# Optimization experiments

Measured on AMD Instinct MI355X. Metric: run time of the kernel, lower is better.

The kernel has to match this reference:

```python
import jax, jax.numpy as jnp
import numpy as np

N = 50000
D = 64
K_POS = 32
K_NEG = 64


def setup_inputs() -> dict:
    key = jax.random.key(0)
    ks = jax.random.split(key, 7)
    return {
        "P": jax.random.normal(ks[0], (N, D), dtype=jnp.float32),
        "W_d": jax.random.normal(ks[1], (D,), dtype=jnp.float32),
        "deg_vec": jax.random.uniform(ks[2], (N,), dtype=jnp.float32),
        "pos_idx": jax.random.randint(ks[3], (N, K_POS), 0, N, dtype=jnp.int32),
        "neg_idx": jax.random.randint(ks[4], (N, K_NEG), 0, N, dtype=jnp.int32),
        "deg_pos_idx": jax.random.randint(ks[5], (N, K_POS), 0, N, dtype=jnp.int32),
        "deg_neg_idx": jax.random.randint(ks[6], (N, K_NEG), 0, N, dtype=jnp.int32),
    }


def _contrast(Z, pos, neg):
    # hamming_dist(zi, zp) = sum_d |zi - zp|  (per node i over its index list)
    Hp = jnp.abs(Z[:, None, :] - Z[pos]).sum(-1)  # [N, K_pos]
    Hn = jnp.abs(Z[:, None, :] - Z[neg]).sum(-1)  # [N, K_neg]
    # softmax_formula: -( mean_p H_pos - log sum_n exp(H_neg) ), summed over nodes
    per_node = Hp.mean(-1) - jax.nn.logsumexp(Hn, axis=-1)
    return -per_node.sum()


def reference(P, W_d, deg_vec, pos_idx, neg_idx, deg_pos_idx, deg_neg_idx):
    Z = jax.nn.sigmoid(P)  # Sigmoid_alt assumed elementwise logistic sigmoid
    L_adj = _contrast(Z, pos_idx, neg_idx)
    L_deg_dist = _contrast(Z, deg_pos_idx, deg_neg_idx)
    # degree_loss: MSE(Z @ W_d, deg_vec)
    L_deg = jnp.mean((Z @ W_d - deg_vec) ** 2)
    return (L_adj, L_deg_dist, L_deg)
```

## Files before the change

kernel.cpp:

```cpp
#include <hip/hip_runtime.h>
#include <stdint.h>

#define NDIM 64
#define KPOS 32
#define KNEG 64

__global__ __launch_bounds__(256) void pe_sig_deg_kernel(
    const float* __restrict__ P,
    const float* __restrict__ Wd,
    const float* __restrict__ deg,
    uint8_t* __restrict__ Zq,
    float* __restrict__ out,
    int N) {
  const int lane = threadIdx.x & 63;
  const int wid  = threadIdx.x >> 6;
  const int nwaves = (gridDim.x * blockDim.x) >> 6;
  int gw = (blockIdx.x * blockDim.x + threadIdx.x) >> 6;

  const float wd = Wd[lane];
  float acc = 0.f;
  for (int i = gw; i < N; i += nwaves) {
    float p = P[(unsigned)i * NDIM + lane];
    float z = 1.f / (1.f + __expf(-p));
    Zq[((unsigned)i << 6) | lane] = (uint8_t)(z * 255.f + 0.5f);
    float dot = z * wd;
    #pragma unroll
    for (int off = 32; off; off >>= 1) dot += __shfl_xor(dot, off);
    float d = dot - deg[i];
    acc += d * d;
  }
  __shared__ float sacc[4];
  if (lane == 0) sacc[wid] = acc;
  __syncthreads();
  if (threadIdx.x == 0) {
    atomicAdd(out + 2, (sacc[0] + sacc[1] + sacc[2] + sacc[3]) * (1.0f / (float)N));
  }
}

__device__ __forceinline__ unsigned sad16(uint4 a, uint4 b, unsigned acc) {
  acc = __builtin_amdgcn_sad_u8(a.x, b.x, acc);
  acc = __builtin_amdgcn_sad_u8(a.y, b.y, acc);
  acc = __builtin_amdgcn_sad_u8(a.z, b.z, acc);
  acc = __builtin_amdgcn_sad_u8(a.w, b.w, acc);
  return acc;
}

struct Idx { int p0, p1, n0, n1, n2, n3, q0, q1, m0, m1, m2, m3; };

__device__ __forceinline__ Idx load_idx(
    const int* __restrict__ pos, const int* __restrict__ neg,
    const int* __restrict__ dpos, const int* __restrict__ dneg,
    unsigned i, int q) {
  Idx d;
  const int* pr = pos  + i * KPOS;
  const int* nr = neg  + i * KNEG;
  const int* qr = dpos + i * KPOS;
  const int* mr = dneg + i * KNEG;
  d.p0 = pr[q]; d.p1 = pr[16 + q];
  d.n0 = nr[q]; d.n1 = nr[16 + q]; d.n2 = nr[32 + q]; d.n3 = nr[48 + q];
  d.q0 = qr[q]; d.q1 = qr[16 + q];
  d.m0 = mr[q]; d.m1 = mr[16 + q]; d.m2 = mr[32 + q]; d.m3 = mr[48 + q];
  return d;
}

__global__ __launch_bounds__(256) void pe_contrast_kernel(
    const uint8_t* __restrict__ Zq,
    const int* __restrict__ pos_idx,
    const int* __restrict__ neg_idx,
    const int* __restrict__ dpos_idx,
    const int* __restrict__ dneg_idx,
    float* __restrict__ out,
    int N) {
  const int lane = threadIdx.x & 63;
  const int q = lane >> 2, c = lane & 3;
  const int wid  = threadIdx.x >> 6;
  const int nwaves = (gridDim.x * blockDim.x) >> 6;
  const int gw = (blockIdx.x * blockDim.x + threadIdx.x) >> 6;

  const unsigned coff = (unsigned)c << 4;
  #define ZROW(j) (*(const uint4*)(Zq + ((((unsigned)(j)) << 6) | coff)))

  float l1 = 0.f, l2 = 0.f;
  unsigned pa1 = 0u, pa2 = 0u;
  const float S = 1.4426950408889634f / 255.f;

  int i = gw;
  Idx cur;
  if (i < N) cur = load_idx(pos_idx, neg_idx, dpos_idx, dneg_idx, (unsigned)i, q);
  while (i < N) {
    const uint4 zi  = ZROW(i);
    const uint4 rp0 = ZROW(cur.p0), rp1 = ZROW(cur.p1);
    const uint4 rn0 = ZROW(cur.n0), rn1 = ZROW(cur.n1);
    const uint4 rn2 = ZROW(cur.n2), rn3 = ZROW(cur.n3);
    const uint4 rq0 = ZROW(cur.q0), rq1 = ZROW(cur.q1);
    const uint4 rm0 = ZROW(cur.m0), rm1 = ZROW(cur.m1);
    const uint4 rm2 = ZROW(cur.m2), rm3 = ZROW(cur.m3);

    const int inext = i + nwaves;
    Idx nxt = cur;
    if (inext < N) nxt = load_idx(pos_idx, neg_idx, dpos_idx, dneg_idx, (unsigned)inext, q);

    pa1 = sad16(rp0, zi, sad16(rp1, zi, pa1));
    pa2 = sad16(rq0, zi, sad16(rq1, zi, pa2));

    int h0 = (int)sad16(rn0, zi, 0u), h1 = (int)sad16(rn1, zi, 0u);
    int h2 = (int)sad16(rn2, zi, 0u), h3 = (int)sad16(rn3, zi, 0u);
    int g0 = (int)sad16(rm0, zi, 0u), g1 = (int)sad16(rm1, zi, 0u);
    int g2 = (int)sad16(rm2, zi, 0u), g3 = (int)sad16(rm3, zi, 0u);

    h0 += __shfl_xor(h0, 1); h1 += __shfl_xor(h1, 1);
    h2 += __shfl_xor(h2, 1); h3 += __shfl_xor(h3, 1);
    g0 += __shfl_xor(g0, 1); g1 += __shfl_xor(g1, 1);
    g2 += __shfl_xor(g2, 1); g3 += __shfl_xor(g3, 1);
    h0 += __shfl_xor(h0, 2); h1 += __shfl_xor(h1, 2);
    h2 += __shfl_xor(h2, 2); h3 += __shfl_xor(h3, 2);
    g0 += __shfl_xor(g0, 2); g1 += __shfl_xor(g1, 2);
    g2 += __shfl_xor(g2, 2); g3 += __shfl_xor(g3, 2);

    float e1 = exp2f((float)h0 * S) + exp2f((float)h1 * S) +
               exp2f((float)h2 * S) + exp2f((float)h3 * S);
    float e2 = exp2f((float)g0 * S) + exp2f((float)g1 * S) +
               exp2f((float)g2 * S) + exp2f((float)g3 * S);
    #pragma unroll
    for (int o = 4; o < 64; o <<= 1) {
      e1 += __shfl_xor(e1, o);
      e2 += __shfl_xor(e2, o);
    }
    l1 += __logf(e1);
    l2 += __logf(e2);

    i = inext;
    cur = nxt;
  }

  int p1s = (int)pa1, p2s = (int)pa2;
  #pragma unroll
  for (int o = 1; o < 64; o <<= 1) { p1s += __shfl_xor(p1s, o); p2s += __shfl_xor(p2s, o); }

  const float pscale = 1.f / (255.f * (float)KPOS);
  const float c1 = l1 - (float)p1s * pscale;
  const float c2 = l2 - (float)p2s * pscale;

  __shared__ float s1[4], s2[4];
  if (lane == 0) { s1[wid] = c1; s2[wid] = c2; }
  __syncthreads();
  if (threadIdx.x == 0) {
    atomicAdd(out + 0, s1[0] + s1[1] + s1[2] + s1[3]);
    atomicAdd(out + 1, s2[0] + s2[1] + s2[2] + s2[3]);
  }
  #undef ZROW
}

extern "C" void kernel_launch(void* const* d_in, const int* in_sizes, int n_in,
                              void* d_out, int out_size, void* d_ws, size_t ws_size,
                              hipStream_t stream) {
  const float* P       = (const float*)d_in[0];
  const float* Wd      = (const float*)d_in[1];
  const float* deg     = (const float*)d_in[2];
  const int*   pos_idx = (const int*)d_in[3];
  const int*   neg_idx = (const int*)d_in[4];
  const int*   dpos    = (const int*)d_in[5];
  const int*   dneg    = (const int*)d_in[6];
  float* out = (float*)d_out;

  const int N = in_sizes[2];
  uint8_t* Zq = (uint8_t*)d_ws;

  hipMemsetAsync(out, 0, (size_t)out_size * sizeof(float), stream);

  pe_sig_deg_kernel<<<2048, 256, 0, stream>>>(P, Wd, deg, Zq, out, N);
  pe_contrast_kernel<<<2048, 256, 0, stream>>>(Zq, pos_idx, neg_idx, dpos, dneg, out, N);
}
```

Before: 111.4 us.

## Double-buffer row gathers across nodes and use ds_swizzle reductions

Restructures the contrast loop so each node's Z-row gathers and the index loads for the node two steps ahead are issued before the current node is computed. The goal is to hide gather latency behind the SAD and exp work. Index loads clamp to N-1 instead of being guarded by branches. The intra-32-lane xor reductions switch from shfl_xor to ds_swizzle bitmask mode, and the sigmoid/degree kernel launches half as many blocks. The extra buffered rows raise VGPR usage and could lower occupancy.

```diff
diff --git a/kernel.cpp b/kernel.cpp
--- a/kernel.cpp
+++ b/kernel.cpp
@@ -4,6 +4,9 @@
 #define NDIM 64
 #define KPOS 32
 #define KNEG 64
+
+#define SWZI(x, pat) __builtin_amdgcn_ds_swizzle((x), (pat))
+#define SWZF(x, pat) __int_as_float(__builtin_amdgcn_ds_swizzle(__float_as_int(x), (pat)))
 
 __global__ __launch_bounds__(256) void pe_sig_deg_kernel(
     const float* __restrict__ P,
@@ -47,20 +50,70 @@
 
 struct Idx { int p0, p1, n0, n1, n2, n3, q0, q1, m0, m1, m2, m3; };
 
-__device__ __forceinline__ Idx load_idx(
+__device__ __forceinline__ Idx load_idx_clamped(
     const int* __restrict__ pos, const int* __restrict__ neg,
     const int* __restrict__ dpos, const int* __restrict__ dneg,
-    unsigned i, int q) {
+    int i, int N, int q) {
+  unsigned u = (unsigned)((i < N) ? i : (N - 1));
   Idx d;
-  const int* pr = pos  + i * KPOS;
-  const int* nr = neg  + i * KNEG;
-  const int* qr = dpos + i * KPOS;
-  const int* mr = dneg + i * KNEG;
+  const int* pr = pos  + u * KPOS;
+  const int* nr = neg  + u * KNEG;
+  const int* qr = dpos + u * KPOS;
+  const int* mr = dneg + u * KNEG;
   d.p0 = pr[q]; d.p1 = pr[16 + q];
   d.n0 = nr[q]; d.n1 = nr[16 + q]; d.n2 = nr[32 + q]; d.n3 = nr[48 + q];
   d.q0 = qr[q]; d.q1 = qr[16 + q];
   d.m0 = mr[q]; d.m1 = mr[16 + q]; d.m2 = mr[32 + q]; d.m3 = mr[48 + q];
   return d;
+}
+
+struct Rows { uint4 z, p0, p1, n0, n1, n2, n3, q0, q1, m0, m1, m2, m3; };
+
+__device__ __forceinline__ Rows gather_rows(const uint8_t* __restrict__ Zq,
+                                            int i, const Idx& d, unsigned coff) {
+  #define ZROW(j) (*(const uint4*)(Zq + ((((unsigned)(j)) << 6) | coff)))
+  Rows r;
+  r.z  = ZROW(i);
+  r.p0 = ZROW(d.p0); r.p1 = ZROW(d.p1);
+  r.n0 = ZROW(d.n0); r.n1 = ZROW(d.n1); r.n2 = ZROW(d.n2); r.n3 = ZROW(d.n3);
+  r.q0 = ZROW(d.q0); r.q1 = ZROW(d.q1);
+  r.m0 = ZROW(d.m0); r.m1 = ZROW(d.m1); r.m2 = ZROW(d.m2); r.m3 = ZROW(d.m3);
+  return r;
+  #undef ZROW
+}
+
+__device__ __forceinline__ void compute_node(const Rows& r,
+    float& l1, float& l2, unsigned& pa1, unsigned& pa2) {
+  const float S = 1.4426950408889634f / 255.f;
+
+  pa1 = sad16(r.p0, r.z, sad16(r.p1, r.z, pa1));
+  pa2 = sad16(r.q0, r.z, sad16(r.q1, r.z, pa2));
+
+  int h0 = (int)sad16(r.n0, r.z, 0u), h1 = (int)sad16(r.n1, r.z, 0u);
+  int h2 = (int)sad16(r.n2, r.z, 0u), h3 = (int)sad16(r.n3, r.z, 0u);
+  int g0 = (int)sad16(r.m0, r.z, 0u), g1 = (int)sad16(r.m1, r.z, 0u);
+  int g2 = (int)sad16(r.m2, r.z, 0u), g3 = (int)sad16(r.m3, r.z, 0u);
+
+  h0 += SWZI(h0, 0x041F); h1 += SWZI(h1, 0x041F);
+  h2 += SWZI(h2, 0x041F); h3 += SWZI(h3, 0x041F);
+  g0 += SWZI(g0, 0x041F); g1 += SWZI(g1, 0x041F);
+  g2 += SWZI(g2, 0x041F); g3 += SWZI(g3, 0x041F);
+  h0 += SWZI(h0, 0x081F); h1 += SWZI(h1, 0x081F);
+  h2 += SWZI(h2, 0x081F); h3 += SWZI(h3, 0x081F);
+  g0 += SWZI(g0, 0x081F); g1 += SWZI(g1, 0x081F);
+  g2 += SWZI(g2, 0x081F); g3 += SWZI(g3, 0x081F);
+
+  float e1 = exp2f((float)h0 * S) + exp2f((float)h1 * S) +
+             exp2f((float)h2 * S) + exp2f((float)h3 * S);
+  float e2 = exp2f((float)g0 * S) + exp2f((float)g1 * S) +
+             exp2f((float)g2 * S) + exp2f((float)g3 * S);
+  e1 += SWZF(e1, 0x101F); e2 += SWZF(e2, 0x101F);
+  e1 += SWZF(e1, 0x201F); e2 += SWZF(e2, 0x201F);
+  e1 += SWZF(e1, 0x401F); e2 += SWZF(e2, 0x401F);
+  e1 += __shfl_xor(e1, 32); e2 += __shfl_xor(e2, 32);
+
+  l1 += __logf(e1);
+  l2 += __logf(e2);
 }
 
 __global__ __launch_bounds__(256) void pe_contrast_kernel(
@@ -74,63 +127,41 @@
   const int lane = threadIdx.x & 63;
   const int q = lane >> 2, c = lane & 3;
   const int wid  = threadIdx.x >> 6;
-  const int nwaves = (gridDim.x * blockDim.x) >> 6;
-  const int gw = (blockIdx.x * blockDim.x + threadIdx.x) >> 6;
-
+  const int nw   = (gridDim.x * blockDim.x) >> 6;
+  const int gw   = (blockIdx.x * blockDim.x + threadIdx.x) >> 6;
   const unsigned coff = (unsigned)c << 4;
-  #define ZROW(j) (*(const uint4*)(Zq + ((((unsigned)(j)) << 6) | coff)))
 
   float l1 = 0.f, l2 = 0.f;
   unsigned pa1 = 0u, pa2 = 0u;
-  const float S = 1.4426950408889634f / 255.f;
 
   int i = gw;
-  Idx cur;
-  if (i < N) cur = load_idx(pos_idx, neg_idx, dpos_idx, dneg_idx, (unsigned)i, q);
-  while (i < N) {
-    const uint4 zi  = ZROW(i);
-    const uint4 rp0 = ZROW(cur.p0), rp1 = ZROW(cur.p1);
-    const uint4 rn0 = ZROW(cur.n0), rn1 = ZROW(cur.n1);
-    const uint4 rn2 = ZROW(cur.n2), rn3 = ZROW(cur.n3);
-    const uint4 rq0 = ZROW(cur.q0), rq1 = ZROW(cur.q1);
-    const uint4 rm0 = ZROW(cur.m0), rm1 = ZROW(cur.m1);
-    const uint4 rm2 = ZROW(cur.m2), rm3 = ZROW(cur.m3);
-
-    const int inext = i + nwaves;
-    Idx nxt = cur;
-    if (inext < N) nxt = load_idx(pos_idx, neg_idx, dpos_idx, dneg_idx, (unsigned)inext, q);
-
-    pa1 = sad16(rp0, zi, sad16(rp1, zi, pa1));
-    pa2 = sad16(rq0, zi, sad16(rq1, zi, pa2));
-
-    int h0 = (int)sad16(rn0, zi, 0u), h1 = (int)sad16(rn1, zi, 0u);
-    int h2 = (int)sad16(rn2, zi, 0u), h3 = (int)sad16(rn3, zi, 0u);
-    int g0 = (int)sad16(rm0, zi, 0u), g1 = (int)sad16(rm1, zi, 0u);
-    int g2 = (int)sad16(rm2, zi, 0u), g3 = (int)sad16(rm3, zi, 0u);
-
-    h0 += __shfl_xor(h0, 1); h1 += __shfl_xor(h1, 1);
-    h2 += __shfl_xor(h2, 1); h3 += __shfl_xor(h3, 1);
-    g0 += __shfl_xor(g0, 1); g1 += __shfl_xor(g1, 1);
-    g2 += __shfl_xor(g2, 1); g3 += __shfl_xor(g3, 1);
-    h0 += __shfl_xor(h0, 2); h1 += __shfl_xor(h1, 2);
-    h2 += __shfl_xor(h2, 2); h3 += __shfl_xor(h3, 2);
-    g0 += __shfl_xor(g0, 2); g1 += __shfl_xor(g1, 2);
-    g2 += __shfl_xor(g2, 2); g3 += __shfl_xor(g3, 2);
-
-    float e1 = exp2f((float)h0 * S) + exp2f((float)h1 * S) +
-               exp2f((float)h2 * S) + exp2f((float)h3 * S);
-    float e2 = exp2f((float)g0 * S) + exp2f((float)g1 * S) +
-               exp2f((float)g2 * S) + exp2f((float)g3 * S);
-    #pragma unroll
-    for (int o = 4; o < 64; o <<= 1) {
-      e1 += __shfl_xor(e1, o);
-      e2 += __shfl_xor(e2, o);
+  if (i < N) {
+    Idx dA = load_idx_clamped(pos_idx, neg_idx, dpos_idx, dneg_idx, i, N, q);
+    Rows rA = gather_rows(Zq, i, dA, coff);
+    int iB = i + nw;
+    Idx dB = load_idx_clamped(pos_idx, neg_idx, dpos_idx, dneg_idx, iB, N, q);
+
+    while (true) {
+      const bool vB = (iB < N);
+      Rows rB;
+      if (vB) rB = gather_rows(Zq, iB, dB, coff);
+      const int iC = iB + nw;
+      Idx dC = load_idx_clamped(pos_idx, neg_idx, dpos_idx, dneg_idx, iC, N, q);
+
+      compute_node(rA, l1, l2, pa1, pa2);
+      if (!vB) break;
+
+      const bool vC = (iC < N);
+      Rows rC;
+      if (vC) rC = gather_rows(Zq, iC, dC, coff);
+      const int iD = iC + nw;
+      Idx dD = load_idx_clamped(pos_idx, neg_idx, dpos_idx, dneg_idx, iD, N, q);
+
+      compute_node(rB, l1, l2, pa1, pa2);
+      if (!vC) break;
+
+      rA = rC; dB = dD; iB = iD;
     }
-    l1 += __logf(e1);
-    l2 += __logf(e2);
-
-    i = inext;
-    cur = nxt;
   }
 
   int p1s = (int)pa1, p2s = (int)pa2;
@@ -148,7 +179,6 @@
     atomicAdd(out + 0, s1[0] + s1[1] + s1[2] + s1[3]);
     atomicAdd(out + 1, s2[0] + s2[1] + s2[2] + s2[3]);
   }
-  #undef ZROW
 }
 
 extern "C" void kernel_launch(void* const* d_in, const int* in_sizes, int n_in,
@@ -168,6 +198,6 @@
 
   hipMemsetAsync(out, 0, (size_t)out_size * sizeof(float), stream);
 
-  pe_sig_deg_kernel<<<2048, 256, 0, stream>>>(P, Wd, deg, Zq, out, N);
+  pe_sig_deg_kernel<<<1024, 256, 0, stream>>>(P, Wd, deg, Zq, out, N);
   pe_contrast_kernel<<<2048, 256, 0, stream>>>(Zq, pos_idx, neg_idx, dpos, dneg, out, N);
 }
```

Result: faster. 101.6 us (-8.8%).
